# Kernel tuning notes

Hardware: AMD Instinct MI355X
Metric: run time of the kernel (lower is better)

The kernel has to match this reference:

```python
import jax, jax.numpy as jnp
import numpy as np

N_STATE = 1024
N_HEAD = 16
HEAD_DIM = N_STATE // N_HEAD


def setup_inputs() -> dict:
    key = jax.random.key(0)
    ks = jax.random.split(key, 8)
    s = 0.02
    return {
        "x": jax.random.normal(ks[0], (4, 1500, N_STATE), dtype=jnp.float32),
        "Wq": jax.random.normal(ks[1], (N_STATE, N_STATE), dtype=jnp.float32) * s,
        "bq": jnp.zeros((N_STATE,), dtype=jnp.float32),
        "Wk": jax.random.normal(ks[2], (N_STATE, N_STATE), dtype=jnp.float32) * s,
        "Wv": jax.random.normal(ks[3], (N_STATE, N_STATE), dtype=jnp.float32) * s,
        "bv": jnp.zeros((N_STATE,), dtype=jnp.float32),
        "Wo": jax.random.normal(ks[4], (N_STATE, N_STATE), dtype=jnp.float32) * s,
        "bo": jnp.zeros((N_STATE,), dtype=jnp.float32),
    }


def reference(x, Wq, bq, Wk, Wv, bv, Wo, bo):
    B, S, _ = x.shape
    scale = HEAD_DIM ** (-0.5)
    # projections (torch Linear: y = x @ W.T + b)
    q = x @ Wq.T + bq
    k = x @ Wk.T
    v = x @ Wv.T + bv
    # [B, H, S, D]
    q = q.reshape(B, S, N_HEAD, HEAD_DIM).transpose(0, 2, 1, 3)
    k = k.reshape(B, S, N_HEAD, HEAD_DIM).transpose(0, 2, 1, 3)
    v = v.reshape(B, S, N_HEAD, HEAD_DIM).transpose(0, 2, 1, 3)
    # scores scaled AFTER the matmul, as in the original (qk * qk_scale)
    qk = jnp.einsum("bhqd,bhkd->bhqk", q, k) * scale
    w = jax.nn.softmax(qk, axis=-1)
    wv = jnp.einsum("bhqk,bhkd->bhqd", w, v)
    wv = wv.transpose(0, 2, 1, 3).reshape(B, S, N_STATE)
    return wv @ Wo.T + bo
```

## Files before the change

kernel.cpp:

```cpp
#include <hip/hip_runtime.h>
#include <stdint.h>

#define S_LEN  1500
#define S_PAD  1536
#define BATCH  4
#define NSTATE 1024
#define NHEAD  16
#define HDIM   64
#define MROWS  6000

typedef __attribute__((ext_vector_type(8)))  short short8;
typedef __attribute__((ext_vector_type(4)))  float floatx4;
typedef __attribute__((ext_vector_type(16))) float floatx16;

__device__ __forceinline__ unsigned short f2bf(float f) {
  union { float f; unsigned int u; } v; v.f = f;
  unsigned int r = v.u + 0x7fffu + ((v.u >> 16) & 1u);
  return (unsigned short)(r >> 16);
}

__device__ __forceinline__ void gld_lds16(const void* g, void* l) {
  __builtin_amdgcn_global_load_lds(
      (const __attribute__((address_space(1))) void*)g,
      (__attribute__((address_space(3))) void*)l, 16, 0, 0);
}

__global__ __launch_bounds__(256) void cvt_all(
    const float* __restrict__ x,  const float* __restrict__ Wq,
    const float* __restrict__ Wk, const float* __restrict__ Wv,
    const float* __restrict__ Wo, unsigned short* __restrict__ dst)
{
  const size_t NX = (size_t)MROWS * NSTATE;
  size_t e = ((size_t)blockIdx.x * 256 + threadIdx.x) * 4;
  const float* src; size_t off;
  if (e < NX) { src = x; off = e; }
  else {
    size_t t = e - NX;
    int wsel = (int)(t >> 20);
    off = t & ((1u << 20) - 1);
    src = (wsel == 0) ? Wq : (wsel == 1) ? Wk : (wsel == 2) ? Wv : Wo;
  }
  float4 v = *(const float4*)(src + off);
  uint2 o;
  o.x = (unsigned int)f2bf(v.x) | ((unsigned int)f2bf(v.y) << 16);
  o.y = (unsigned int)f2bf(v.z) | ((unsigned int)f2bf(v.w) << 16);
  *(uint2*)(dst + e) = o;
}

template <bool F32OUT>
__device__ __forceinline__ void gemm128_bt(
    const unsigned short* __restrict__ X,
    const unsigned short* __restrict__ W,
    const float* __restrict__ bias,
    void* __restrict__ Yv,
    int m0, int n0)
{
  __shared__ unsigned short As[2][128 * 32];
  __shared__ unsigned short Bs[2][128 * 32];

  const int tid  = threadIdx.x;
  const int lane = tid & 63;
  const int wid  = tid >> 6;
  const int wm   = (wid & 1) * 64;
  const int wn   = (wid >> 1) * 64;
  const int l15  = lane & 15;
  const int l4   = lane >> 4;

  floatx4 acc[4][4];
#pragma unroll
  for (int i = 0; i < 4; ++i)
#pragma unroll
    for (int j = 0; j < 4; ++j)
      acc[i][j] = (floatx4){0.f, 0.f, 0.f, 0.f};

  const int srow  = tid >> 2;
  const int scolb = (tid & 3) * 16;

  const char* xrp[2];
  const char* wrp[2];
#pragma unroll
  for (int r = 0; r < 2; ++r) {
    int arow = m0 + r * 64 + srow;
    if (arow > MROWS - 1) arow = MROWS - 1;
    xrp[r] = (const char*)X + (size_t)arow * NSTATE * 2 + scolb;
    int brow = n0 + r * 64 + srow;
    wrp[r] = (const char*)W + (size_t)brow * NSTATE * 2 + scolb;
  }

  for (int k0 = 0; k0 < NSTATE; k0 += 64) {
    __syncthreads();
#pragma unroll
    for (int h = 0; h < 2; ++h) {
      int kb = (k0 + h * 32) * 2;
#pragma unroll
      for (int r = 0; r < 2; ++r) {
        gld_lds16(xrp[r] + kb, (char*)As[h] + r * 4096 + wid * 1024);
        gld_lds16(wrp[r] + kb, (char*)Bs[h] + r * 4096 + wid * 1024);
      }
    }
    __syncthreads();

#pragma unroll
    for (int h = 0; h < 2; ++h) {
      short8 a[4], b[4];
#pragma unroll
      for (int i = 0; i < 4; ++i)
        a[i] = *(const short8*)(As[h] + (wm + i * 16 + l15) * 32 + l4 * 8);
#pragma unroll
      for (int j = 0; j < 4; ++j)
        b[j] = *(const short8*)(Bs[h] + (wn + j * 16 + l15) * 32 + l4 * 8);
#pragma unroll
      for (int i = 0; i < 4; ++i)
#pragma unroll
        for (int j = 0; j < 4; ++j)
          acc[i][j] = __builtin_amdgcn_mfma_f32_16x16x32_bf16(a[i], b[j], acc[i][j], 0, 0, 0);
    }
  }

#pragma unroll
  for (int j = 0; j < 4; ++j) {
    int ng = n0 + wn + j * 16 + l15;
    float bias_v = bias ? bias[ng] : 0.f;
#pragma unroll
    for (int i = 0; i < 4; ++i) {
      int mgb = m0 + wm + i * 16 + l4 * 4;
#pragma unroll
      for (int r = 0; r < 4; ++r) {
        int mg = mgb + r;
        if (mg < MROWS) {
          float val = acc[i][j][r] + bias_v;
          if (F32OUT) ((float*)Yv)[(size_t)mg * NSTATE + ng] = val;
          else        ((unsigned short*)Yv)[(size_t)mg * NSTATE + ng] = f2bf(val);
        }
      }
    }
  }
}

__global__ __launch_bounds__(256) void proj_qkv(
    const unsigned short* __restrict__ X,
    const unsigned short* __restrict__ Wq, const unsigned short* __restrict__ Wk,
    const unsigned short* __restrict__ Wv,
    const float* __restrict__ bq, const float* __restrict__ bv,
    unsigned short* __restrict__ q, unsigned short* __restrict__ k,
    unsigned short* __restrict__ v)
{
  const int z = blockIdx.z;
  const unsigned short* W = (z == 0) ? Wq : (z == 1) ? Wk : Wv;
  const float* bias       = (z == 0) ? bq : (z == 1) ? (const float*)nullptr : bv;
  unsigned short* Y       = (z == 0) ? q  : (z == 1) ? k  : v;
  gemm128_bt<false>(X, W, bias, Y, blockIdx.x * 128, blockIdx.y * 128);
}

__global__ __launch_bounds__(256) void proj_o(
    const unsigned short* __restrict__ X, const unsigned short* __restrict__ W,
    const float* __restrict__ bias, float* __restrict__ Y)
{
  gemm128_bt<true>(X, W, bias, Y, blockIdx.x * 128, blockIdx.y * 128);
}

__global__ __launch_bounds__(256) void vtrans(
    const unsigned short* __restrict__ v, unsigned short* __restrict__ vt)
{
  __shared__ unsigned short T[64][72];
  const int tid = threadIdx.x;
  const int st = blockIdx.x * 64, h = blockIdx.y, b = blockIdx.z;
#pragma unroll
  for (int rr = 0; rr < 2; ++rr) {
    int sl = rr * 32 + (tid >> 3);
    int dl = (tid & 7) * 8;
    int s  = st + sl;
    uint4 val = make_uint4(0u, 0u, 0u, 0u);
    if (s < S_LEN)
      val = *(const uint4*)&v[((size_t)b * S_LEN + s) * NSTATE + h * HDIM + dl];
    *(uint4*)&T[sl][dl] = val;
  }
  __syncthreads();
#pragma unroll
  for (int rr = 0; rr < 2; ++rr) {
    int dl = rr * 32 + (tid >> 3);
    int s0 = (tid & 7) * 8;
    unsigned short tmp[8];
#pragma unroll
    for (int j2 = 0; j2 < 8; ++j2) tmp[j2] = T[s0 + j2][dl];
    *(uint4*)&vt[(((size_t)b * NHEAD + h) * HDIM + dl) * S_PAD + st + s0] =
        *(const uint4*)tmp;
  }
}

#define C1 0.180336879f

__global__ __launch_bounds__(256, 4) void attn32t(
    const unsigned short* __restrict__ Q, const unsigned short* __restrict__ K,
    const unsigned short* __restrict__ VT, unsigned short* __restrict__ O)
{
  __shared__ unsigned short SMEM[16384];
  unsigned short* Ks  = SMEM;
  unsigned short* Vts = SMEM + 8192;
  unsigned short* Os  = SMEM;

  const int tid  = threadIdx.x;
  const int lane = tid & 63;
  const int w    = tid >> 6;
  const int l31  = lane & 31;
  const int lhi  = lane >> 5;
  const int qt = blockIdx.x, h = blockIdx.y, b = blockIdx.z;
  const size_t base  = ((size_t)b * S_LEN) * NSTATE + h * HDIM;
  const size_t vbase = (((size_t)b * NHEAD + h) * HDIM) * S_PAD;

  short8 qf[4];
  {
    int qrow = qt * 128 + w * 32 + l31;
    if (qrow > S_LEN - 1) qrow = S_LEN - 1;
    const unsigned short* qp = Q + base + (size_t)qrow * NSTATE;
#pragma unroll
    for (int c = 0; c < 4; ++c)
      qf[c] = *(const short8*)(qp + c * 16 + lhi * 8);
  }

  floatx16 oacc[2];
  oacc[0] = (floatx16)(0.f);
  oacc[1] = (floatx16)(0.f);
  float l_loc = 0.f;

  for (int t = 0; t < 12; ++t) {
    __syncthreads();
#pragma unroll
    for (int qq = 0; qq < 4; ++qq) {
      int row  = (w * 4 + qq) * 8 + (lane >> 3);
      int logc = (lane & 7) ^ (row & 7);
      int s = t * 128 + row; if (s > S_LEN - 1) s = S_LEN - 1;
      gld_lds16(&K[base + (size_t)s * NSTATE + logc * 8],
                (char*)Ks + (w * 4 + qq) * 1024);
    }
#pragma unroll
    for (int qq = 0; qq < 4; ++qq) {
      int d    = (w * 4 + qq) * 4 + (lane >> 4);
      int logc = (lane & 15) ^ (d & 7);
      gld_lds16(&VT[vbase + (size_t)d * S_PAD + t * 128 + logc * 8],
                (char*)Vts + (w * 4 + qq) * 1024);
    }
    __syncthreads();

#pragma unroll
    for (int kvt = 0; kvt < 4; ++kvt) {
      floatx16 sacc = (floatx16)(0.f);
#pragma unroll
      for (int c = 0; c < 4; ++c) {
        int row  = kvt * 32 + l31;
        int phys = (c * 2 + lhi) ^ (row & 7);
        short8 ak = *(const short8*)(Ks + row * 64 + phys * 8);
        sacc = __builtin_amdgcn_mfma_f32_32x32x16_bf16(ak, qf[c], sacc, 0, 0, 0);
      }

      if (t == 11 && kvt >= 2) {
        if (kvt == 3) {
#pragma unroll
          for (int r = 0; r < 16; ++r) sacc[r] = -3.0e38f;
        } else {
#pragma unroll
          for (int r = 12; r < 16; ++r) sacc[r] = lhi ? -3.0e38f : sacc[r];
        }
      }

      unsigned int pu[16];
#pragma unroll
      for (int r = 0; r < 16; ++r) {
        float p = exp2f(sacc[r] * C1);
        unsigned int u = __float_as_uint(p) & 0xffff0000u;
        l_loc += __uint_as_float(u);
        pu[r] = u;
      }
      unsigned int pk[8], ex[8];
#pragma unroll
      for (int i = 0; i < 8; ++i)
        pk[i] = __builtin_amdgcn_perm(pu[2 * i + 1], pu[2 * i], 0x07060302);
#pragma unroll
      for (int i = 0; i < 8; ++i)
        ex[i] = __shfl_xor((unsigned int)pk[i], 32, 64);

      int4 f0i, f1i;
      f0i.x = lhi ? ex[2] : pk[0];
      f0i.y = lhi ? ex[3] : pk[1];
      f0i.z = lhi ? pk[2] : ex[0];
      f0i.w = lhi ? pk[3] : ex[1];
      f1i.x = lhi ? ex[6] : pk[4];
      f1i.y = lhi ? ex[7] : pk[5];
      f1i.z = lhi ? pk[6] : ex[4];
      f1i.w = lhi ? pk[7] : ex[5];
      short8 f0 = *(short8*)&f0i;
      short8 f1 = *(short8*)&f1i;

#pragma unroll
      for (int dt = 0; dt < 2; ++dt) {
        int d = dt * 32 + l31;
        int p0 = ((kvt * 4 + 0) + lhi) ^ (d & 7);
        int p1 = ((kvt * 4 + 2) + lhi) ^ (d & 7);
        short8 av0 = *(const short8*)(Vts + d * 128 + p0 * 8);
        short8 av1 = *(const short8*)(Vts + d * 128 + p1 * 8);
        oacc[dt] = __builtin_amdgcn_mfma_f32_32x32x16_bf16(av0, f0, oacc[dt], 0, 0, 0);
        oacc[dt] = __builtin_amdgcn_mfma_f32_32x32x16_bf16(av1, f1, oacc[dt], 0, 0, 0);
      }
    }
  }

  float l_all = l_loc + __shfl_xor(l_loc, 32, 64);
  float inv = 1.f / l_all;

  __syncthreads();
#pragma unroll
  for (int dt = 0; dt < 2; ++dt)
#pragma unroll
    for (int g = 0; g < 4; ++g) {
      int d0 = dt * 32 + g * 8 + lhi * 4;
      float v0 = oacc[dt][4 * g + 0] * inv;
      float v1 = oacc[dt][4 * g + 1] * inv;
      float v2 = oacc[dt][4 * g + 2] * inv;
      float v3 = oacc[dt][4 * g + 3] * inv;
      uint2 pk2;
      pk2.x = (unsigned int)f2bf(v0) | ((unsigned int)f2bf(v1) << 16);
      pk2.y = (unsigned int)f2bf(v2) | ((unsigned int)f2bf(v3) << 16);
      *(uint2*)&Os[(w * 32 + l31) * 72 + d0] = pk2;
    }
  __syncthreads();
#pragma unroll
  for (int pass = 0; pass < 4; ++pass) {
    int e = pass * 256 + tid;
    int row = e >> 3, ch = e & 7;
    int s = qt * 128 + row;
    if (s < S_LEN)
      *(uint4*)&O[base + (size_t)s * NSTATE + ch * 8] = *(const uint4*)&Os[row * 72 + ch * 8];
  }
}

extern "C" void kernel_launch(void* const* d_in, const int* in_sizes, int n_in,
                              void* d_out, int out_size, void* d_ws, size_t ws_size,
                              hipStream_t stream) {
  const float* x  = (const float*)d_in[0];
  const float* Wq = (const float*)d_in[1];
  const float* bq = (const float*)d_in[2];
  const float* Wk = (const float*)d_in[3];
  const float* Wv = (const float*)d_in[4];
  const float* bv = (const float*)d_in[5];
  const float* Wo = (const float*)d_in[6];
  const float* bo = (const float*)d_in[7];
  float* out = (float*)d_out;

  const size_t NX = (size_t)MROWS * NSTATE;
  const size_t NW = (size_t)NSTATE * NSTATE;

  unsigned short* xb  = (unsigned short*)d_ws;
  unsigned short* Wqb = xb  + NX;
  unsigned short* Wkb = Wqb + NW;
  unsigned short* Wvb = Wkb + NW;
  unsigned short* Wob = Wvb + NW;
  unsigned short* q   = Wob + NW;
  unsigned short* k   = q + NX;
  unsigned short* v   = k + NX;
  unsigned short* vt  = v + NX;
  unsigned short* wv  = xb;

  dim3 blk(256);
  const size_t n4_total = (NX + 4 * NW) / 4;
  cvt_all<<<dim3((int)(n4_total / 256)), blk, 0, stream>>>(x, Wq, Wk, Wv, Wo, xb);
  proj_qkv<<<dim3(47, 8, 3), blk, 0, stream>>>(xb, Wqb, Wkb, Wvb, bq, bv, q, k, v);
  vtrans<<<dim3(24, NHEAD, BATCH), blk, 0, stream>>>(v, vt);
  attn32t<<<dim3(12, NHEAD, BATCH), blk, 0, stream>>>(q, k, vt, wv);
  proj_o<<<dim3(47, 8, 1), blk, 0, stream>>>(wv, Wob, bo, out);
}
```

Baseline: 275.5 us.

## Fold softmax scale into Q projection, MFMA row sums, XCD-aware block remap

Multiplies the Q projection output by the log2-scaled softmax constant so the attention loop calls exp2 directly on the scores. Packs probabilities with a hardware bf16 pack instruction and computes the softmax denominator with an extra MFMA against a ones vector instead of scalar accumulation plus a cross-lane shuffle. Remaps 1D block indices in all three GEMM/attention kernels so that consecutive blocks spread across the 8 XCDs in contiguous chunks, aiming to improve L2 locality. Rounding Q after scaling and packing with a different rounding mode slightly changes numerics.

```diff
diff --git a/kernel.cpp b/kernel.cpp
--- a/kernel.cpp
+++ b/kernel.cpp
@@ -8,6 +8,7 @@
 #define NHEAD  16
 #define HDIM   64
 #define MROWS  6000
+#define C1 0.180336879f
 
 typedef __attribute__((ext_vector_type(8)))  short short8;
 typedef __attribute__((ext_vector_type(4)))  float floatx4;
@@ -53,7 +54,7 @@
     const unsigned short* __restrict__ W,
     const float* __restrict__ bias,
     void* __restrict__ Yv,
-    int m0, int n0)
+    int m0, int n0, float oscale)
 {
   __shared__ unsigned short As[2][128 * 32];
   __shared__ unsigned short Bs[2][128 * 32];
@@ -128,7 +129,7 @@
       for (int r = 0; r < 4; ++r) {
         int mg = mgb + r;
         if (mg < MROWS) {
-          float val = acc[i][j][r] + bias_v;
+          float val = (acc[i][j][r] + bias_v) * oscale;
           if (F32OUT) ((float*)Yv)[(size_t)mg * NSTATE + ng] = val;
           else        ((unsigned short*)Yv)[(size_t)mg * NSTATE + ng] = f2bf(val);
         }
@@ -145,18 +146,27 @@
     unsigned short* __restrict__ q, unsigned short* __restrict__ k,
     unsigned short* __restrict__ v)
 {
-  const int z = blockIdx.z;
+  const int id  = blockIdx.x;
+  const int sid = (id & 7) * 141 + (id >> 3);
+  const int z   = sid / 376;
+  const int rem = sid - z * 376;
+  const int m0  = (rem >> 3) * 128;
+  const int n0  = (rem & 7) * 128;
+
   const unsigned short* W = (z == 0) ? Wq : (z == 1) ? Wk : Wv;
   const float* bias       = (z == 0) ? bq : (z == 1) ? (const float*)nullptr : bv;
   unsigned short* Y       = (z == 0) ? q  : (z == 1) ? k  : v;
-  gemm128_bt<false>(X, W, bias, Y, blockIdx.x * 128, blockIdx.y * 128);
+  const float osc         = (z == 0) ? C1 : 1.0f;
+  gemm128_bt<false>(X, W, bias, Y, m0, n0, osc);
 }
 
 __global__ __launch_bounds__(256) void proj_o(
     const unsigned short* __restrict__ X, const unsigned short* __restrict__ W,
     const float* __restrict__ bias, float* __restrict__ Y)
 {
-  gemm128_bt<true>(X, W, bias, Y, blockIdx.x * 128, blockIdx.y * 128);
+  const int id  = blockIdx.x;
+  const int sid = (id & 7) * 47 + (id >> 3);
+  gemm128_bt<true>(X, W, bias, Y, (sid >> 3) * 128, (sid & 7) * 128, 1.0f);
 }
 
 __global__ __launch_bounds__(256) void vtrans(
@@ -188,8 +198,6 @@
   }
 }
 
-#define C1 0.180336879f
-
 __global__ __launch_bounds__(256, 4) void attn32t(
     const unsigned short* __restrict__ Q, const unsigned short* __restrict__ K,
     const unsigned short* __restrict__ VT, unsigned short* __restrict__ O)
@@ -204,7 +212,14 @@
   const int w    = tid >> 6;
   const int l31  = lane & 31;
   const int lhi  = lane >> 5;
-  const int qt = blockIdx.x, h = blockIdx.y, b = blockIdx.z;
+
+  const int id  = blockIdx.x;
+  const int sid = (id & 7) * 96 + (id >> 3);
+  const int qt  = sid % 12;
+  const int hb  = sid / 12;
+  const int h   = hb & 15;
+  const int b   = hb >> 4;
+
   const size_t base  = ((size_t)b * S_LEN) * NSTATE + h * HDIM;
   const size_t vbase = (((size_t)b * NHEAD + h) * HDIM) * S_PAD;
 
@@ -218,10 +233,14 @@
       qf[c] = *(const short8*)(qp + c * 16 + lhi * 8);
   }
 
+  short8 ones8;
+#pragma unroll
+  for (int i = 0; i < 8; ++i) ones8[i] = (short)0x3F80;
+
   floatx16 oacc[2];
   oacc[0] = (floatx16)(0.f);
   oacc[1] = (floatx16)(0.f);
-  float l_loc = 0.f;
+  floatx16 lacc = (floatx16)(0.f);
 
   for (int t = 0; t < 12; ++t) {
     __syncthreads();
@@ -263,18 +282,15 @@
         }
       }
 
-      unsigned int pu[16];
-#pragma unroll
-      for (int r = 0; r < 16; ++r) {
-        float p = exp2f(sacc[r] * C1);
-        unsigned int u = __float_as_uint(p) & 0xffff0000u;
-        l_loc += __uint_as_float(u);
-        pu[r] = u;
-      }
       unsigned int pk[8], ex[8];
 #pragma unroll
-      for (int i = 0; i < 8; ++i)
-        pk[i] = __builtin_amdgcn_perm(pu[2 * i + 1], pu[2 * i], 0x07060302);
+      for (int i = 0; i < 8; ++i) {
+        float plo = exp2f(sacc[2 * i]);
+        float phi = exp2f(sacc[2 * i + 1]);
+        unsigned int rr;
+        asm("v_cvt_pk_bf16_f32 %0, %1, %2" : "=v"(rr) : "v"(plo), "v"(phi));
+        pk[i] = rr;
+      }
 #pragma unroll
       for (int i = 0; i < 8; ++i)
         ex[i] = __shfl_xor((unsigned int)pk[i], 32, 64);
@@ -291,6 +307,9 @@
       short8 f0 = *(short8*)&f0i;
       short8 f1 = *(short8*)&f1i;
 
+      lacc = __builtin_amdgcn_mfma_f32_32x32x16_bf16(ones8, f0, lacc, 0, 0, 0);
+      lacc = __builtin_amdgcn_mfma_f32_32x32x16_bf16(ones8, f1, lacc, 0, 0, 0);
+
 #pragma unroll
       for (int dt = 0; dt < 2; ++dt) {
         int d = dt * 32 + l31;
@@ -304,8 +323,7 @@
     }
   }
 
-  float l_all = l_loc + __shfl_xor(l_loc, 32, 64);
-  float inv = 1.f / l_all;
+  float inv = 1.f / lacc[0];
 
   __syncthreads();
 #pragma unroll
@@ -363,8 +381,8 @@
   dim3 blk(256);
   const size_t n4_total = (NX + 4 * NW) / 4;
   cvt_all<<<dim3((int)(n4_total / 256)), blk, 0, stream>>>(x, Wq, Wk, Wv, Wo, xb);
-  proj_qkv<<<dim3(47, 8, 3), blk, 0, stream>>>(xb, Wqb, Wkb, Wvb, bq, bv, q, k, v);
+  proj_qkv<<<dim3(1128), blk, 0, stream>>>(xb, Wqb, Wkb, Wvb, bq, bv, q, k, v);
   vtrans<<<dim3(24, NHEAD, BATCH), blk, 0, stream>>>(v, vt);
-  attn32t<<<dim3(12, NHEAD, BATCH), blk, 0, stream>>>(q, k, vt, wv);
-  proj_o<<<dim3(47, 8, 1), blk, 0, stream>>>(wv, Wob, bo, out);
-}
+  attn32t<<<dim3(768), blk, 0, stream>>>(q, k, vt, wv);
+  proj_o<<<dim3(376), blk, 0, stream>>>(wv, Wob, bo, out);
+}
```

Result: faster. 255.7 us (-7.2%).
